# Kernel optimization log

Hardware: AMD Instinct MI355X
Metric: run time of the kernel (lower is better)

The kernel has to match this reference:

```python
import jax, jax.numpy as jnp
import numpy as np

B, T, D, H, F = 4, 1024, 1024, 16, 4096
DH = D // H
EPS = 1e-5


def _ln(x, g, b):
    m = jnp.mean(x, axis=-1, keepdims=True)
    v = jnp.mean((x - m) ** 2, axis=-1, keepdims=True)
    return (x - m) * jax.lax.rsqrt(v + EPS) * g + b


def setup_inputs() -> dict:
    key = jax.random.key(0)
    ks = jax.random.split(key, 16)
    w = lambda k, s: jax.random.normal(k, s, jnp.float32) * 0.02
    return {
        "x": jax.random.normal(ks[0], (B, T, D), jnp.float32),
        "spatial_encoding": jax.random.normal(ks[1], (B, T, D), jnp.float32),
        "edge_encoding": jax.random.normal(ks[2], (B, T, D), jnp.float32),
        "ln1_g": jnp.ones((D,), jnp.float32), "ln1_b": jnp.zeros((D,), jnp.float32),
        "Wq": w(ks[3], (D, D)), "bq": jnp.zeros((D,), jnp.float32),
        "Wk": w(ks[4], (D, D)), "bk": jnp.zeros((D,), jnp.float32),
        "Wv": w(ks[5], (D, D)), "bv": jnp.zeros((D,), jnp.float32),
        "Wo": w(ks[6], (D, D)), "bo": jnp.zeros((D,), jnp.float32),
        "ln2_g": jnp.ones((D,), jnp.float32), "ln2_b": jnp.zeros((D,), jnp.float32),
        "W1": w(ks[7], (D, F)), "b1": jnp.zeros((F,), jnp.float32),
        "W2": w(ks[8], (F, D)), "b2": jnp.zeros((D,), jnp.float32),
        "lnb_g": jnp.ones((D,), jnp.float32), "lnb_b": jnp.zeros((D,), jnp.float32),
    }


def reference(x, spatial_encoding, edge_encoding, ln1_g, ln1_b,
              Wq, bq, Wk, bk, Wv, bv, Wo, bo, ln2_g, ln2_b,
              W1, b1, W2, b2, lnb_g, lnb_b):
    # pre-attention LayerNorm, residual taken post-norm (as in the torch code)
    x = _ln(x, ln1_g, ln1_b)
    residual = x
    # graph attention with spatial/edge score biases
    q = (x @ Wq + bq).reshape(B, T, H, DH)
    k = (x @ Wk + bk).reshape(B, T, H, DH)
    v = (x @ Wv + bv).reshape(B, T, H, DH)
    kb = k + spatial_encoding.reshape(B, T, H, DH) + edge_encoding.reshape(B, T, H, DH)
    scores = jnp.einsum('bthd,bshd->bhts', q, kb) / jnp.sqrt(jnp.float32(DH))
    attn = jax.nn.softmax(scores, axis=-1)  # (B, H, T, T)
    ctx = jnp.einsum('bhts,bshd->bthd', attn, v).reshape(B, T, D)
    x = ctx @ Wo + bo + residual
    x = _ln(x, ln2_g, ln2_b)
    # bottleneck FFN with residual + LayerNorm
    h = jax.nn.gelu(x @ W1 + b1) @ W2 + b2
    x = _ln(x + h, lnb_g, lnb_b)
    return (x, attn)
```

## Files before the change

kernel.cpp:

```cpp
#include <hip/hip_runtime.h>
#include <hip/hip_bf16.h>
#include <hip/hip_fp16.h>
#include <math.h>

#define B_ 4
#define T_ 1024
#define D_ 1024
#define H_ 16
#define DH_ 64
#define F_ 4096
#define BT_ (B_ * T_)
#define BTD ((size_t)B_ * T_ * D_)

typedef short bf16x8 __attribute__((ext_vector_type(8)));
typedef _Float16 f16x8 __attribute__((ext_vector_type(8)));
typedef float f32x4 __attribute__((ext_vector_type(4)));

__device__ __forceinline__ unsigned short f2b(float f) {
  __hip_bfloat16 h = __float2bfloat16(f);
  return *reinterpret_cast<unsigned short*>(&h);
}
__device__ __forceinline__ unsigned short f2h(float f) {
  __half h = __float2half(f);
  return *reinterpret_cast<unsigned short*>(&h);
}

__device__ __forceinline__ void gload16(const unsigned short* g, unsigned short* l) {
  __builtin_amdgcn_global_load_lds(
      (const __attribute__((address_space(1))) unsigned int*)(const void*)g,
      (__attribute__((address_space(3))) unsigned int*)(void*)l, 16, 0, 0);
}

__device__ __forceinline__ float gelu_f(float x) {
  float z2 = 1.5957691216057308f * (x + 0.044715f * x * x * x);
  return x / (1.0f + __expf(-z2));
}

__device__ __forceinline__ float blk_sum256(float v, float* s4) {
#pragma unroll
  for (int off = 32; off > 0; off >>= 1) v += __shfl_down(v, off);
  if ((threadIdx.x & 63) == 0) s4[threadIdx.x >> 6] = v;
  __syncthreads();
  float t = s4[0] + s4[1] + s4[2] + s4[3];
  __syncthreads();
  return t;
}

__global__ __launch_bounds__(256) void ln_rows(
    const float* __restrict__ in, const float* __restrict__ in2,
    const float* __restrict__ g, const float* __restrict__ bb,
    float* __restrict__ outf, unsigned short* __restrict__ outb) {
  __shared__ float s4[4];
  const size_t base = (size_t)blockIdx.x * D_;
  const int t = threadIdx.x;
  float4 v = ((const float4*)(in + base))[t];
  if (in2) {
    float4 w = ((const float4*)(in2 + base))[t];
    v.x += w.x; v.y += w.y; v.z += w.z; v.w += w.w;
  }
  float mean = blk_sum256(v.x + v.y + v.z + v.w, s4) * (1.0f / D_);
  float dx = v.x - mean, dy = v.y - mean, dz = v.z - mean, dw = v.w - mean;
  float var = blk_sum256(dx * dx + dy * dy + dz * dz + dw * dw, s4) * (1.0f / D_);
  float rstd = rsqrtf(var + 1e-5f);
  float4 gv = ((const float4*)g)[t];
  float4 bv = ((const float4*)bb)[t];
  float4 o;
  o.x = dx * rstd * gv.x + bv.x;
  o.y = dy * rstd * gv.y + bv.y;
  o.z = dz * rstd * gv.z + bv.z;
  o.w = dw * rstd * gv.w + bv.w;
  if (outf) ((float4*)(outf + base))[t] = o;
  if (outb) {
    unsigned short o4[4] = {f2b(o.x), f2b(o.y), f2b(o.z), f2b(o.w)};
    *(uint2*)(&outb[base + (size_t)t * 4]) = *(uint2*)o4;
  }
}

__global__ __launch_bounds__(256) void tcast_t(
    const float* __restrict__ in, unsigned short* __restrict__ out, int R, int C) {
  __shared__ unsigned short tile[32][33];
  const int c0 = blockIdx.x * 32, r0 = blockIdx.y * 32;
  const int col = threadIdx.x & 31, rq = threadIdx.x >> 5;
#pragma unroll
  for (int i = 0; i < 4; ++i) {
    int r = rq + i * 8;
    tile[r][col] = f2b(in[(size_t)(r0 + r) * C + c0 + col]);
  }
  __syncthreads();
#pragma unroll
  for (int i = 0; i < 4; ++i) {
    int r = rq + i * 8;
    out[(size_t)(c0 + r) * R + r0 + col] = tile[col][r];
  }
}

__global__ __launch_bounds__(256) void tcast4(
    const float* w0, const float* w1, const float* w2, const float* w3,
    unsigned short* o0, unsigned short* o1, unsigned short* o2, unsigned short* o3) {
  __shared__ unsigned short tile[32][33];
  const float* in = blockIdx.z == 0 ? w0 : blockIdx.z == 1 ? w1 : blockIdx.z == 2 ? w2 : w3;
  unsigned short* out = blockIdx.z == 0 ? o0 : blockIdx.z == 1 ? o1 : blockIdx.z == 2 ? o2 : o3;
  const int c0 = blockIdx.x * 32, r0 = blockIdx.y * 32;
  const int col = threadIdx.x & 31, rq = threadIdx.x >> 5;
#pragma unroll
  for (int i = 0; i < 4; ++i) {
    int r = rq + i * 8;
    tile[r][col] = f2b(in[(size_t)(r0 + r) * D_ + c0 + col]);
  }
  __syncthreads();
#pragma unroll
  for (int i = 0; i < 4; ++i) {
    int r = rq + i * 8;
    out[(size_t)(c0 + r) * D_ + r0 + col] = tile[col][r];
  }
}

__global__ __launch_bounds__(256, 4) void attn_fused(
    const unsigned short* __restrict__ qh, const unsigned short* __restrict__ kh,
    const unsigned short* __restrict__ vt, float* __restrict__ attn,
    unsigned short* __restrict__ ctxb) {
  __shared__ __align__(16) unsigned short L[5 * 4096];
  unsigned short* const R0 = L;
  unsigned short* const R1 = L + 4096;
  unsigned short* const R2 = L + 2 * 4096;
  unsigned short* const R3 = L + 3 * 4096;
  unsigned short* const R4 = L + 4 * 4096;
  const int tid = threadIdx.x;
  const int l = tid & 63, w = tid >> 6;
  const int wm = w >> 1, wn = w & 1;
  const int lk = l >> 4, lr = l & 15;
  const int bh = blockIdx.x, b = bh >> 4, h = bh & 15;
  const int tt = blockIdx.y;
  const unsigned short* Qg = qh + (size_t)b * T_ * D_ + h * DH_ + (size_t)tt * 64 * D_;
  const unsigned short* Kg = kh + (size_t)b * T_ * D_ + h * DH_;
  const unsigned short* Vg = vt + (size_t)bh * 64 * T_;

  const int ar = tid >> 3, ac = tid & 7;
  const int aswz = ((ac ^ (ar & 7)) << 3);

  auto stageK = [&](int st, unsigned short* buf) {
#pragma unroll
    for (int i = 0; i < 2; ++i)
      gload16(Kg + (size_t)(st * 64 + ar + 32 * i) * D_ + aswz, &buf[(size_t)(i * 256 + tid) * 8]);
  };
  auto stageV = [&](int st, unsigned short* buf) {
#pragma unroll
    for (int i = 0; i < 2; ++i)
      gload16(Vg + (size_t)(ar + 32 * i) * T_ + st * 64 + aswz, &buf[(size_t)(i * 256 + tid) * 8]);
  };

#pragma unroll
  for (int i = 0; i < 2; ++i)
    gload16(Qg + (size_t)(ar + 32 * i) * D_ + aswz, &R0[(size_t)(i * 256 + tid) * 8]);
  stageK(0, R1);
  asm volatile("s_waitcnt vmcnt(2)" ::: "memory");
  __builtin_amdgcn_s_barrier();
  __builtin_amdgcn_sched_barrier(0);
  f16x8 qf[2][2];
#pragma unroll
  for (int mi = 0; mi < 2; ++mi) {
    const int row = wm * 32 + mi * 16 + lr;
#pragma unroll
    for (int kk = 0; kk < 2; ++kk)
      qf[mi][kk] = *(const f16x8*)&R0[row * 64 + (((kk * 4 + lk) ^ (row & 7)) << 3)];
  }

  float lsum[2][4] = {};

  for (int st = 0; st < 16; ++st) {
    asm volatile("s_waitcnt vmcnt(0) lgkmcnt(0)" ::: "memory");
    __builtin_amdgcn_s_barrier();
    __builtin_amdgcn_sched_barrier(0);
    if (st + 1 < 16) stageK(st + 1, ((st + 1) & 1) ? R2 : R1);
    __builtin_amdgcn_sched_barrier(0);
    const unsigned short* Kb = (st & 1) ? R2 : R1;
    f16x8 kf[2][2];
#pragma unroll
    for (int ni = 0; ni < 2; ++ni) {
      const int row = wn * 32 + ni * 16 + lr;
#pragma unroll
      for (int kk = 0; kk < 2; ++kk)
        kf[ni][kk] = *(const f16x8*)&Kb[row * 64 + (((kk * 4 + lk) ^ (row & 7)) << 3)];
    }
    f32x4 acc[2][2] = {};
#pragma unroll
    for (int kk = 0; kk < 2; ++kk)
#pragma unroll
      for (int mi = 0; mi < 2; ++mi)
#pragma unroll
        for (int ni = 0; ni < 2; ++ni)
          acc[mi][ni] = __builtin_amdgcn_mfma_f32_16x16x32_f16(
              qf[mi][kk], kf[ni][kk], acc[mi][ni], 0, 0, 0);
#pragma unroll
    for (int mi = 0; mi < 2; ++mi)
#pragma unroll
      for (int r = 0; r < 4; ++r)
        lsum[mi][r] += __expf(acc[mi][0][r] * 0.125f) + __expf(acc[mi][1][r] * 0.125f);
  }
#pragma unroll
  for (int mi = 0; mi < 2; ++mi)
#pragma unroll
    for (int r = 0; r < 4; ++r) {
      float v = lsum[mi][r];
      v += __shfl_xor(v, 1); v += __shfl_xor(v, 2);
      v += __shfl_xor(v, 4); v += __shfl_xor(v, 8);
      lsum[mi][r] = v;
    }

  float* sL = (float*)R4;
  if (lr == 0) {
#pragma unroll
    for (int mi = 0; mi < 2; ++mi)
#pragma unroll
      for (int r = 0; r < 4; ++r)
        sL[wn * 64 + wm * 32 + mi * 16 + lk * 4 + r] = lsum[mi][r];
  }
  asm volatile("s_waitcnt lgkmcnt(0)" ::: "memory");
  __builtin_amdgcn_s_barrier();
  __builtin_amdgcn_sched_barrier(0);
  float rl[2][4];
#pragma unroll
  for (int mi = 0; mi < 2; ++mi)
#pragma unroll
    for (int r = 0; r < 4; ++r) {
      const int row = wm * 32 + mi * 16 + lk * 4 + r;
      rl[mi][r] = 1.0f / (sL[row] + sL[64 + row]);
    }
  asm volatile("s_waitcnt lgkmcnt(0)" ::: "memory");
  __builtin_amdgcn_sched_barrier(0);
  stageK(0, R1);
  stageV(0, R2);
  __builtin_amdgcn_sched_barrier(0);

  float* Cg = attn + (size_t)bh * T_ * T_;
  f32x4 cacc[2][2] = {};
  for (int st = 0; st < 16; ++st) {
    if (st == 0) asm volatile("s_waitcnt vmcnt(0) lgkmcnt(0)" ::: "memory");
    else         asm volatile("s_waitcnt vmcnt(16) lgkmcnt(0)" ::: "memory");
    __builtin_amdgcn_s_barrier();
    __builtin_amdgcn_sched_barrier(0);
    if (st + 1 < 16) {
      stageK(st + 1, ((st + 1) & 1) ? R0 : R1);
      stageV(st + 1, ((st + 1) & 1) ? R3 : R2);
    }
    __builtin_amdgcn_sched_barrier(0);
    const unsigned short* Kb = (st & 1) ? R0 : R1;
    const unsigned short* Vb = (st & 1) ? R3 : R2;
    f16x8 kf[2][2], vf[2][2];
#pragma unroll
    for (int ni = 0; ni < 2; ++ni) {
      const int row = wn * 32 + ni * 16 + lr;
#pragma unroll
      for (int kk = 0; kk < 2; ++kk) {
        kf[ni][kk] = *(const f16x8*)&Kb[row * 64 + (((kk * 4 + lk) ^ (row & 7)) << 3)];
        vf[ni][kk] = *(const f16x8*)&Vb[row * 64 + (((kk * 4 + lk) ^ (row & 7)) << 3)];
      }
    }
    f32x4 acc[2][2] = {};
#pragma unroll
    for (int kk = 0; kk < 2; ++kk)
#pragma unroll
      for (int mi = 0; mi < 2; ++mi)
#pragma unroll
        for (int ni = 0; ni < 2; ++ni)
          acc[mi][ni] = __builtin_amdgcn_mfma_f32_16x16x32_f16(
              qf[mi][kk], kf[ni][kk], acc[mi][ni], 0, 0, 0);
#pragma unroll
    for (int mi = 0; mi < 2; ++mi) {
      const int trow = wm * 32 + mi * 16 + lk * 4;
#pragma unroll
      for (int ni = 0; ni < 2; ++ni) {
        const int scol = wn * 32 + ni * 16 + lr;
#pragma unroll
        for (int r = 0; r < 4; ++r) {
          const int t = trow + r;
          float p = __expf(acc[mi][ni][r] * 0.125f) * rl[mi][r];
          __builtin_nontemporal_store(
              p, &Cg[(size_t)(tt * 64 + t) * T_ + (st * 64 + scol)]);
          R4[t * 64 + (scol ^ ((t & 7) << 3))] = f2h(p);
        }
      }
    }
    asm volatile("s_waitcnt lgkmcnt(0)" ::: "memory");
    __builtin_amdgcn_s_barrier();
    __builtin_amdgcn_sched_barrier(0);
#pragma unroll
    for (int kk = 0; kk < 2; ++kk) {
      f16x8 af[2];
#pragma unroll
      for (int mi = 0; mi < 2; ++mi) {
        const int row = wm * 32 + mi * 16 + lr;
        af[mi] = *(const f16x8*)&R4[row * 64 + (((kk * 4 + lk) ^ (row & 7)) << 3)];
      }
#pragma unroll
      for (int mi = 0; mi < 2; ++mi)
#pragma unroll
        for (int ni = 0; ni < 2; ++ni)
          cacc[mi][ni] = __builtin_amdgcn_mfma_f32_16x16x32_f16(
              af[mi], vf[ni][kk], cacc[mi][ni], 0, 0, 0);
    }
  }

  unsigned short* Cb = ctxb + (size_t)b * T_ * D_ + h * DH_;
  const int crow0 = tt * 64 + wm * 32 + lk * 4;
  const int ccol0 = wn * 32 + lr;
#pragma unroll
  for (int mi = 0; mi < 2; ++mi)
#pragma unroll
    for (int ni = 0; ni < 2; ++ni)
#pragma unroll
      for (int r = 0; r < 4; ++r)
        Cb[(size_t)(crow0 + mi * 16 + r) * D_ + ccol0 + ni * 16] = f2b(cacc[mi][ni][r]);
}

template <int BN, int EPI, bool WF32, bool W16, bool FP16 = false, bool DB = false,
          int NT = 256>
__global__ __launch_bounds__(NT) void gemm_nt(
    const unsigned short* __restrict__ A, int lda,
    const unsigned short* __restrict__ Bm, int ldb,
    float* __restrict__ Cf, unsigned short* __restrict__ Cb, int ldc,
    const float* __restrict__ bias, const float* __restrict__ r1,
    const float* __restrict__ r2, float scale, int K) {
  constexpr int BM = 128, BK = 64;
  constexpr int WAVES = NT / 64;
  constexpr int WNC = WAVES / 2;
  constexpr int WN = BN / WNC;
  constexpr int FN = WN / 16;
  constexpr int NB = DB ? 4 : 1;
  constexpr int RS = NT / 8;
  constexpr int AI = BM / RS, BI = BN / RS;
  __shared__ __align__(16) unsigned short As[NB][BM * BK];
  __shared__ __align__(16) unsigned short Bs[NB][BN * BK];
  const int tid = threadIdx.x;
  const int l = tid & 63;
  const int w = tid >> 6;
  const int wm = w / WNC, wn = w % WNC;
  const int lr = l & 15, lk = l >> 4;
  const unsigned short* Ab = A + (size_t)blockIdx.y * BM * lda;
  const unsigned short* Bb = Bm + (size_t)blockIdx.x * BN * ldb;

  const int ar = tid >> 3;
  const int ac = tid & 7;
  const int aswz = ((ac ^ (ar & 7)) << 3);

  f32x4 acc[4][FN] = {};

  auto stage = [&](int buf, int k0) {
#pragma unroll
    for (int i = 0; i < AI; ++i)
      gload16(Ab + (size_t)(ar + RS * i) * lda + k0 + aswz, &As[buf][(size_t)(i * NT + tid) * 8]);
#pragma unroll
    for (int i = 0; i < BI; ++i)
      gload16(Bb + (size_t)(ar + RS * i) * ldb + k0 + aswz, &Bs[buf][(size_t)(i * NT + tid) * 8]);
  };
  auto compute = [&](int buf) {
    bf16x8 af[4][2], bfr[FN][2];
#pragma unroll
    for (int mi = 0; mi < 4; ++mi) {
      const int row = wm * 64 + mi * 16 + lr;
#pragma unroll
      for (int kk = 0; kk < 2; ++kk)
        af[mi][kk] = *(const bf16x8*)&As[buf][row * BK + (((kk * 4 + lk) ^ (row & 7)) << 3)];
    }
#pragma unroll
    for (int ni = 0; ni < FN; ++ni) {
      const int row = wn * WN + ni * 16 + lr;
#pragma unroll
      for (int kk = 0; kk < 2; ++kk)
        bfr[ni][kk] = *(const bf16x8*)&Bs[buf][row * BK + (((kk * 4 + lk) ^ (row & 7)) << 3)];
    }
#pragma unroll
    for (int kk = 0; kk < 2; ++kk)
#pragma unroll
      for (int mi = 0; mi < 4; ++mi)
#pragma unroll
        for (int ni = 0; ni < FN; ++ni)
          acc[mi][ni] = __builtin_amdgcn_mfma_f32_16x16x32_bf16(
              af[mi][kk], bfr[ni][kk], acc[mi][ni], 0, 0, 0);
  };

  if constexpr (DB) {
    const int nt = K / BK;
    stage(0, 0);
    stage(1, BK);
    stage(2, 2 * BK);
    for (int t = 0; t < nt; ++t) {
      const int rem = nt - 1 - t;
      if constexpr (AI + BI == 8) {
        if (rem >= 2)      asm volatile("s_waitcnt vmcnt(16)" ::: "memory");
        else if (rem == 1) asm volatile("s_waitcnt vmcnt(8)" ::: "memory");
        else               asm volatile("s_waitcnt vmcnt(0)" ::: "memory");
      } else {
        if (rem >= 2)      asm volatile("s_waitcnt vmcnt(8)" ::: "memory");
        else if (rem == 1) asm volatile("s_waitcnt vmcnt(4)" ::: "memory");
        else               asm volatile("s_waitcnt vmcnt(0)" ::: "memory");
      }
      __builtin_amdgcn_s_barrier();
      __builtin_amdgcn_sched_barrier(0);
      if (t + 3 < nt) stage((t + 3) & 3, (t + 3) * BK);
      compute(t & 3);
    }
  } else {
    for (int k0 = 0; k0 < K; k0 += BK) {
      stage(0, k0);
      __syncthreads();
      compute(0);
      __syncthreads();
    }
  }

  const int crow0 = blockIdx.y * BM + wm * 64 + lk * 4;
  const int ccol0 = blockIdx.x * BN + wn * WN + lr;
  if constexpr (EPI == 5) {
#pragma unroll
    for (int mi = 0; mi < 4; ++mi)
#pragma unroll
      for (int ni = 0; ni < FN; ++ni) {
        const int row0 = crow0 + mi * 16;
        const int col = ccol0 + ni * 16;
        unsigned short __attribute__((aligned(8))) p4[4];
#pragma unroll
        for (int r = 0; r < 4; ++r) p4[r] = f2h(acc[mi][ni][r] + bias[col]);
        const int bidx = row0 >> 10, t0 = row0 & 1023;
        const int hh = col >> 6, j = col & 63;
        *(uint2*)&Cb[(((size_t)bidx * 16 + hh) * 64 + j) * T_ + t0] = *(uint2*)p4;
      }
  } else {
#pragma unroll
    for (int mi = 0; mi < 4; ++mi)
#pragma unroll
      for (int ni = 0; ni < FN; ++ni)
#pragma unroll
        for (int r = 0; r < 4; ++r) {
          const int row = crow0 + mi * 16 + r;
          const int col = ccol0 + ni * 16;
          float v = acc[mi][ni][r] * scale;
          if (EPI != 3) v += bias[col];
          if (EPI == 1) v = gelu_f(v);
          const size_t off = (size_t)row * ldc + col;
          if (EPI == 2) v += r1[off];
          if (EPI == 4) v += r1[off] + r2[off];
          if (WF32) Cf[off] = v;
          if (W16) Cb[off] = FP16 ? f2h(v) : f2b(v);
        }
  }
}

__global__ __launch_bounds__(256) void gemm_qkv(
    const unsigned short* __restrict__ A, const unsigned short* __restrict__ Wt,
    const float* __restrict__ bq, const float* __restrict__ bk,
    const float* __restrict__ bv, const float* __restrict__ sp,
    const float* __restrict__ ed, unsigned short* __restrict__ q_h,
    unsigned short* __restrict__ kb_h, unsigned short* __restrict__ vt) {
  constexpr int BM = 128, BN = 128, BK = 64, K = 1024;
  __shared__ __align__(16) unsigned short As[BM * BK];
  __shared__ __align__(16) unsigned short Bs[BN * BK];
  const int tid = threadIdx.x;
  const int l = tid & 63, w = tid >> 6;
  const int wm = w >> 1, wn = w & 1;
  const int lr = l & 15, lk = l >> 4;
  const unsigned short* Ab = A + (size_t)blockIdx.y * BM * D_;
  const unsigned short* Bb = Wt + (size_t)blockIdx.x * BN * D_;
  const int ar = tid >> 3, ac = tid & 7;
  const int aswz = ((ac ^ (ar & 7)) << 3);

  f32x4 acc[4][4] = {};
  for (int k0 = 0; k0 < K; k0 += BK) {
#pragma unroll
    for (int i = 0; i < 4; ++i) {
      gload16(Ab + (size_t)(ar + 32 * i) * D_ + k0 + aswz, &As[(size_t)(i * 256 + tid) * 8]);
      gload16(Bb + (size_t)(ar + 32 * i) * D_ + k0 + aswz, &Bs[(size_t)(i * 256 + tid) * 8]);
    }
    __syncthreads();
    bf16x8 af[4][2], bfr[4][2];
#pragma unroll
    for (int mi = 0; mi < 4; ++mi) {
      const int row = wm * 64 + mi * 16 + lr;
#pragma unroll
      for (int kk = 0; kk < 2; ++kk)
        af[mi][kk] = *(const bf16x8*)&As[row * BK + (((kk * 4 + lk) ^ (row & 7)) << 3)];
    }
#pragma unroll
    for (int ni = 0; ni < 4; ++ni) {
      const int row = wn * 64 + ni * 16 + lr;
#pragma unroll
      for (int kk = 0; kk < 2; ++kk)
        bfr[ni][kk] = *(const bf16x8*)&Bs[row * BK + (((kk * 4 + lk) ^ (row & 7)) << 3)];
    }
#pragma unroll
    for (int kk = 0; kk < 2; ++kk)
#pragma unroll
      for (int mi = 0; mi < 4; ++mi)
#pragma unroll
        for (int ni = 0; ni < 4; ++ni)
          acc[mi][ni] = __builtin_amdgcn_mfma_f32_16x16x32_bf16(
              af[mi][kk], bfr[ni][kk], acc[mi][ni], 0, 0, 0);
    __syncthreads();
  }

  const int seg = blockIdx.x >> 3;
  const float* bias = seg == 0 ? bq : seg == 1 ? bk : bv;
  const int crow0 = blockIdx.y * BM + wm * 64 + lk * 4;
  const int ccol0 = blockIdx.x * BN + wn * 64 + lr;
  if (seg == 2) {
#pragma unroll
    for (int mi = 0; mi < 4; ++mi)
#pragma unroll
      for (int ni = 0; ni < 4; ++ni) {
        const int row0 = crow0 + mi * 16;
        const int col = (ccol0 + ni * 16) & 1023;
        unsigned short __attribute__((aligned(8))) p4[4];
#pragma unroll
        for (int r = 0; r < 4; ++r) p4[r] = f2h(acc[mi][ni][r] + bias[col]);
        const int bidx = row0 >> 10, t0 = row0 & 1023;
        const int hh = col >> 6, j = col & 63;
        *(uint2*)&vt[(((size_t)bidx * 16 + hh) * 64 + j) * T_ + t0] = *(uint2*)p4;
      }
  } else {
    unsigned short* out = seg == 0 ? q_h : kb_h;
#pragma unroll
    for (int mi = 0; mi < 4; ++mi)
#pragma unroll
      for (int ni = 0; ni < 4; ++ni)
#pragma unroll
        for (int r = 0; r < 4; ++r) {
          const int row = crow0 + mi * 16 + r;
          const int col = (ccol0 + ni * 16) & 1023;
          float v = acc[mi][ni][r] + bias[col];
          const size_t off = (size_t)row * D_ + col;
          if (seg == 1) v += sp[off] + ed[off];
          out[off] = f2h(v);
        }
  }
}

extern "C" void kernel_launch(void* const* d_in, const int* in_sizes, int n_in,
                              void* d_out, int out_size, void* d_ws, size_t ws_size,
                              hipStream_t stream) {
  const float* x    = (const float*)d_in[0];
  const float* sp   = (const float*)d_in[1];
  const float* ed   = (const float*)d_in[2];
  const float* ln1g = (const float*)d_in[3];
  const float* ln1b = (const float*)d_in[4];
  const float* Wq   = (const float*)d_in[5];
  const float* bq   = (const float*)d_in[6];
  const float* Wk   = (const float*)d_in[7];
  const float* bk   = (const float*)d_in[8];
  const float* Wv   = (const float*)d_in[9];
  const float* bvv  = (const float*)d_in[10];
  const float* Wo   = (const float*)d_in[11];
  const float* bo   = (const float*)d_in[12];
  const float* ln2g = (const float*)d_in[13];
  const float* ln2b = (const float*)d_in[14];
  const float* W1   = (const float*)d_in[15];
  const float* b1   = (const float*)d_in[16];
  const float* W2   = (const float*)d_in[17];
  const float* b2   = (const float*)d_in[18];
  const float* lnbg = (const float*)d_in[19];
  const float* lnbb = (const float*)d_in[20];

  float* out_x = (float*)d_out;
  float* attn  = out_x + BTD;
  float* tt    = out_x;

  const size_t MB = 1 << 20;
  char* wsb = (char*)d_ws;
  float*          xn    = (float*)(wsb);
  unsigned short* xn_b  = (unsigned short*)(wsb + 16 * MB);
  unsigned short* WqT   = (unsigned short*)(wsb + 24 * MB);
  unsigned short* WkT   = (unsigned short*)(wsb + 26 * MB);
  unsigned short* WvT   = (unsigned short*)(wsb + 28 * MB);
  unsigned short* WoT   = (unsigned short*)(wsb + 30 * MB);
  unsigned short* W1T   = (unsigned short*)(wsb + 32 * MB);
  unsigned short* W2T   = (unsigned short*)(wsb + 40 * MB);
  unsigned short* q_h   = (unsigned short*)(wsb + 48 * MB);
  unsigned short* kb_h  = (unsigned short*)(wsb + 56 * MB);
  unsigned short* vt    = (unsigned short*)(wsb + 80 * MB);
  unsigned short* ctx_b = xn_b;
  unsigned short* h1_b  = (unsigned short*)(wsb + 48 * MB);
  float*          h2    = (float*)(wsb + 80 * MB);
  float*          y     = xn;
  unsigned short* y_b   = xn_b;

  dim3 blk(256);
  dim3 blk512(512);
  dim3 g_dd(8, 32);

  ln_rows<<<BT_, blk, 0, stream>>>(x, nullptr, ln1g, ln1b, xn, xn_b);
  tcast4<<<dim3(32, 32, 4), blk, 0, stream>>>(Wq, Wk, Wv, Wo, WqT, WkT, WvT, WoT);
  tcast_t<<<dim3(128, 32), blk, 0, stream>>>(W1, W1T, 1024, 4096);
  tcast_t<<<dim3(32, 128), blk, 0, stream>>>(W2, W2T, 4096, 1024);
  gemm_qkv<<<dim3(24, 32), blk, 0, stream>>>(
      xn_b, WqT, bq, bk, bvv, sp, ed, q_h, kb_h, vt);
  attn_fused<<<dim3(64, 16), blk, 0, stream>>>(q_h, kb_h, vt, attn, ctx_b);
  gemm_nt<128, 2, true, false, false, true, 512><<<g_dd, blk512, 0, stream>>>(
      ctx_b, D_, WoT, D_, tt, nullptr, D_, bo, xn, nullptr, 1.f, D_);
  ln_rows<<<BT_, blk, 0, stream>>>(tt, nullptr, ln2g, ln2b, y, y_b);
  gemm_nt<128, 1, false, true><<<dim3(32, 32), blk, 0, stream>>>(
      y_b, D_, W1T, D_, nullptr, h1_b, F_, b1, nullptr, nullptr, 1.f, D_);
  gemm_nt<128, 2, true, false, false, true, 512><<<g_dd, blk512, 0, stream>>>(
      h1_b, F_, W2T, F_, h2, nullptr, D_, b2, y, nullptr, 1.f, F_);
  ln_rows<<<BT_, blk, 0, stream>>>(h2, nullptr, lnbg, lnbb, out_x, nullptr);
}
```

Baseline: 341.9 us.

## Give each attention wave whole 16-row strips to drop the P-tile barrier

Repartitions the fused attention kernel's waves from a 2x2 grid of 32x32 tiles to four waves that each own 16 full rows of the 64x64 score tile. Because each wave now writes and then reads only its own rows of the fp16 P buffer in LDS, the workgroup barrier between softmax and the PV MFMAs becomes a per-wave lgkmcnt wait. MFMA blocks are also wrapped in s_setprio raises. In exchange each wave reads all 64 K and V rows from LDS every step, which doubles LDS fragment traffic for K and V.

New measurement: 345.8 us. About the same (+1.1%).

```diff
diff --git a/kernel.cpp b/kernel.cpp
--- a/kernel.cpp
+++ b/kernel.cpp
@@ -232,8 +232,21 @@
   stageV(0, R2);
   __builtin_amdgcn_sched_barrier(0);
 
+  f16x8 qfB[2];
+  float rlB[4];
+  if (w & 1) {
+    qfB[0] = qf[1][0]; qfB[1] = qf[1][1];
+#pragma unroll
+    for (int r = 0; r < 4; ++r) rlB[r] = rl[1][r];
+  } else {
+    qfB[0] = qf[0][0]; qfB[1] = qf[0][1];
+#pragma unroll
+    for (int r = 0; r < 4; ++r) rlB[r] = rl[0][r];
+  }
+  unsigned short* const Pw = R4;
+
   float* Cg = attn + (size_t)bh * T_ * T_;
-  f32x4 cacc[2][2] = {};
+  f32x4 cacc[4] = {};
   for (int st = 0; st < 16; ++st) {
     if (st == 0) asm volatile("s_waitcnt vmcnt(0) lgkmcnt(0)" ::: "memory");
     else         asm volatile("s_waitcnt vmcnt(16) lgkmcnt(0)" ::: "memory");
@@ -246,71 +259,55 @@
     __builtin_amdgcn_sched_barrier(0);
     const unsigned short* Kb = (st & 1) ? R0 : R1;
     const unsigned short* Vb = (st & 1) ? R3 : R2;
-    f16x8 kf[2][2], vf[2][2];
-#pragma unroll
-    for (int ni = 0; ni < 2; ++ni) {
-      const int row = wn * 32 + ni * 16 + lr;
-#pragma unroll
-      for (int kk = 0; kk < 2; ++kk) {
-        kf[ni][kk] = *(const f16x8*)&Kb[row * 64 + (((kk * 4 + lk) ^ (row & 7)) << 3)];
-        vf[ni][kk] = *(const f16x8*)&Vb[row * 64 + (((kk * 4 + lk) ^ (row & 7)) << 3)];
+    f32x4 acc[4] = {};
+    __builtin_amdgcn_s_setprio(1);
+#pragma unroll
+    for (int ni = 0; ni < 4; ++ni) {
+      const int row = ni * 16 + lr;
+      const f16x8 kf0 = *(const f16x8*)&Kb[row * 64 + (((0 + lk) ^ (row & 7)) << 3)];
+      const f16x8 kf1 = *(const f16x8*)&Kb[row * 64 + (((4 + lk) ^ (row & 7)) << 3)];
+      acc[ni] = __builtin_amdgcn_mfma_f32_16x16x32_f16(qfB[0], kf0, acc[ni], 0, 0, 0);
+      acc[ni] = __builtin_amdgcn_mfma_f32_16x16x32_f16(qfB[1], kf1, acc[ni], 0, 0, 0);
+    }
+    __builtin_amdgcn_s_setprio(0);
+#pragma unroll
+    for (int ni = 0; ni < 4; ++ni) {
+      const int scol = ni * 16 + lr;
+#pragma unroll
+      for (int r = 0; r < 4; ++r) {
+        const int t = w * 16 + lk * 4 + r;
+        float p = __expf(acc[ni][r] * 0.125f) * rlB[r];
+        __builtin_nontemporal_store(
+            p, &Cg[(size_t)(tt * 64 + t) * T_ + (st * 64 + scol)]);
+        Pw[t * 64 + (scol ^ ((t & 7) << 3))] = f2h(p);
       }
     }
-    f32x4 acc[2][2] = {};
-#pragma unroll
-    for (int kk = 0; kk < 2; ++kk)
-#pragma unroll
-      for (int mi = 0; mi < 2; ++mi)
-#pragma unroll
-        for (int ni = 0; ni < 2; ++ni)
-          acc[mi][ni] = __builtin_amdgcn_mfma_f32_16x16x32_f16(
-              qf[mi][kk], kf[ni][kk], acc[mi][ni], 0, 0, 0);
-#pragma unroll
-    for (int mi = 0; mi < 2; ++mi) {
-      const int trow = wm * 32 + mi * 16 + lk * 4;
-#pragma unroll
-      for (int ni = 0; ni < 2; ++ni) {
-        const int scol = wn * 32 + ni * 16 + lr;
-#pragma unroll
-        for (int r = 0; r < 4; ++r) {
-          const int t = trow + r;
-          float p = __expf(acc[mi][ni][r] * 0.125f) * rl[mi][r];
-          __builtin_nontemporal_store(
-              p, &Cg[(size_t)(tt * 64 + t) * T_ + (st * 64 + scol)]);
-          R4[t * 64 + (scol ^ ((t & 7) << 3))] = f2h(p);
-        }
+    asm volatile("s_waitcnt lgkmcnt(0)" ::: "memory");
+    __builtin_amdgcn_sched_barrier(0);
+    {
+      const int prow = w * 16 + lr;
+      const f16x8 af0 = *(const f16x8*)&Pw[prow * 64 + (((0 + lk) ^ (prow & 7)) << 3)];
+      const f16x8 af1 = *(const f16x8*)&Pw[prow * 64 + (((4 + lk) ^ (prow & 7)) << 3)];
+      __builtin_amdgcn_s_setprio(1);
+#pragma unroll
+      for (int ni = 0; ni < 4; ++ni) {
+        const int row = ni * 16 + lr;
+        const f16x8 vf0 = *(const f16x8*)&Vb[row * 64 + (((0 + lk) ^ (row & 7)) << 3)];
+        const f16x8 vf1 = *(const f16x8*)&Vb[row * 64 + (((4 + lk) ^ (row & 7)) << 3)];
+        cacc[ni] = __builtin_amdgcn_mfma_f32_16x16x32_f16(af0, vf0, cacc[ni], 0, 0, 0);
+        cacc[ni] = __builtin_amdgcn_mfma_f32_16x16x32_f16(af1, vf1, cacc[ni], 0, 0, 0);
       }
-    }
-    asm volatile("s_waitcnt lgkmcnt(0)" ::: "memory");
-    __builtin_amdgcn_s_barrier();
-    __builtin_amdgcn_sched_barrier(0);
-#pragma unroll
-    for (int kk = 0; kk < 2; ++kk) {
-      f16x8 af[2];
-#pragma unroll
-      for (int mi = 0; mi < 2; ++mi) {
-        const int row = wm * 32 + mi * 16 + lr;
-        af[mi] = *(const f16x8*)&R4[row * 64 + (((kk * 4 + lk) ^ (row & 7)) << 3)];
-      }
-#pragma unroll
-      for (int mi = 0; mi < 2; ++mi)
-#pragma unroll
-        for (int ni = 0; ni < 2; ++ni)
-          cacc[mi][ni] = __builtin_amdgcn_mfma_f32_16x16x32_f16(
-              af[mi], vf[ni][kk], cacc[mi][ni], 0, 0, 0);
+      __builtin_amdgcn_s_setprio(0);
     }
   }
 
   unsigned short* Cb = ctxb + (size_t)b * T_ * D_ + h * DH_;
-  const int crow0 = tt * 64 + wm * 32 + lk * 4;
-  const int ccol0 = wn * 32 + lr;
-#pragma unroll
-  for (int mi = 0; mi < 2; ++mi)
-#pragma unroll
-    for (int ni = 0; ni < 2; ++ni)
-#pragma unroll
-      for (int r = 0; r < 4; ++r)
-        Cb[(size_t)(crow0 + mi * 16 + r) * D_ + ccol0 + ni * 16] = f2b(cacc[mi][ni][r]);
+  const int crow0 = tt * 64 + w * 16 + lk * 4;
+#pragma unroll
+  for (int ni = 0; ni < 4; ++ni)
+#pragma unroll
+    for (int r = 0; r < 4; ++r)
+      Cb[(size_t)(crow0 + r) * D_ + ni * 16 + lr] = f2b(cacc[ni][r]);
 }
 
 template <int BN, int EPI, bool WF32, bool W16, bool FP16 = false, bool DB = false,
```
